# Kernel optimization log

Hardware: AMD Instinct MI355X
Metric: run time of the kernel (lower is better)

## Reference

```python
import jax, jax.numpy as jnp
import numpy as np
from jax import lax


def setup_inputs() -> dict:
    key = jax.random.key(0)
    x = jax.random.normal(key, (16, 3, 1024, 1024), dtype=jnp.float32)
    return {"x": x, "kernel_size": 7}


def _box_conv(x, kernel, pad):
    # x: (B,1,H,W), kernel: (1,1,k,k); 'same' spatial conv
    return lax.conv_general_dilated(
        x, kernel,
        window_strides=(1, 1),
        padding=[(pad, pad), (pad, pad)],
        dimension_numbers=("NCHW", "OIHW", "NCHW"),
    )


def reference(x, kernel_size):
    k = kernel_size
    pad = k // 2
    # ConvertToLuminance: for 4D input, x.dim()==4 -> channel mean (not RGB weights)
    lum = jnp.mean(x, axis=1, keepdims=True)  # (B,1,H,W)
    kernel = jnp.ones((1, 1, k, k), dtype=x.dtype) / (k * k)
    mean = _box_conv(lum, kernel, pad)
    sqr_mean = _box_conv(lum * lum, kernel, pad)
    var = sqr_mean - mean * mean
    return var
```

## Files before the change

### kernel.cpp

```cpp
#include <hip/hip_runtime.h>

#define Wd 1024
#define Hd 1024
#define SH 16
#define ITER (SH + 6)

__global__ __launch_bounds__(256, 4)
void lvm_stream(const float* __restrict__ x, float* __restrict__ out) {
    __shared__ __align__(16) float L[2][Wd + 8];

    const int b    = blockIdx.y;
    const int row0 = blockIdx.x * SH;
    const int tid  = threadIdx.x;
    const int c0   = tid * 4;

    const float* x0 = x + (size_t)b * 3 * Hd * Wd;
    const float* x1 = x0 + (size_t)Hd * Wd;
    const float* x2 = x1 + (size_t)Hd * Wd;
    float*       ob = out + (size_t)b * Hd * Wd;

    if (tid < 4) {
        L[0][tid] = 0.f; L[0][Wd + 4 + tid] = 0.f;
        L[1][tid] = 0.f; L[1][Wd + 4 + tid] = 0.f;
    }

    float4 ring1[7], ring2[7];

#pragma unroll
    for (int i = 0; i < ITER; ++i) {
        const int ri = row0 - 3 + i;
        float4 lum4 = make_float4(0.f, 0.f, 0.f, 0.f);
        if (ri >= 0 && ri < Hd) {
            size_t o = (size_t)ri * Wd + c0;
            float4 a = *(const float4*)(x0 + o);
            float4 g = *(const float4*)(x1 + o);
            float4 c = *(const float4*)(x2 + o);
            lum4.x = (a.x + g.x + c.x) * (1.f / 3.f);
            lum4.y = (a.y + g.y + c.y) * (1.f / 3.f);
            lum4.z = (a.z + g.z + c.z) * (1.f / 3.f);
            lum4.w = (a.w + g.w + c.w) * (1.f / 3.f);
        }
        float* Lr = L[i & 1];
        *(float4*)(Lr + 4 + c0) = lum4;
        __syncthreads();

        float4 va = *(const float4*)(Lr + c0);
        float4 vb = *(const float4*)(Lr + c0 + 4);
        float4 vc = *(const float4*)(Lr + c0 + 8);
        float v1 = va.y, v2 = va.z, v3 = va.w;
        float v4 = vb.x, v5 = vb.y, v6 = vb.z, v7 = vb.w;
        float v8 = vc.x, v9 = vc.y, v10 = vc.z;

        float s1a = v1 + v2 + v3 + v4 + v5 + v6 + v7;
        float s1b = s1a - v1 + v8;
        float s1c = s1b - v2 + v9;
        float s1d = s1c - v3 + v10;

        float q1 = v1 * v1, q2 = v2 * v2, q3 = v3 * v3, q4 = v4 * v4;
        float q5 = v5 * v5, q6 = v6 * v6, q7 = v7 * v7, q8 = v8 * v8;
        float q9 = v9 * v9, q10 = v10 * v10;
        float s2a = q1 + q2 + q3 + q4 + q5 + q6 + q7;
        float s2b = s2a - q1 + q8;
        float s2c = s2b - q2 + q9;
        float s2d = s2c - q3 + q10;

        ring1[i % 7] = make_float4(s1a, s1b, s1c, s1d);
        ring2[i % 7] = make_float4(s2a, s2b, s2c, s2d);

        if (i >= 6) {
            float4 t1 = ring1[0], t2 = ring2[0];
#pragma unroll
            for (int k = 1; k < 7; ++k) {
                t1.x += ring1[k].x; t1.y += ring1[k].y;
                t1.z += ring1[k].z; t1.w += ring1[k].w;
                t2.x += ring2[k].x; t2.y += ring2[k].y;
                t2.z += ring2[k].z; t2.w += ring2[k].w;
            }
            const float inv = 1.f / 49.f;
            float4 r;
            float mx = t1.x * inv, my = t1.y * inv, mz = t1.z * inv, mw = t1.w * inv;
            r.x = t2.x * inv - mx * mx;
            r.y = t2.y * inv - my * my;
            r.z = t2.z * inv - mz * mz;
            r.w = t2.w * inv - mw * mw;
            const int ro = row0 + i - 6;
            *(float4*)(ob + (size_t)ro * Wd + c0) = r;
        }
    }
}

extern "C" void kernel_launch(void* const* d_in, const int* in_sizes, int n_in,
                              void* d_out, int out_size, void* d_ws, size_t ws_size,
                              hipStream_t stream) {
    const float* x = (const float*)d_in[0];
    float* out = (float*)d_out;
    dim3 grid(Hd / SH, 16);
    lvm_stream<<<grid, dim3(256), 0, stream>>>(x, out);
}
```

Measured before the change: 302.3 us.

## Replace shared-memory row staging with wave shuffles and running vertical sum

Removes the LDS double buffer and per-row __syncthreads by getting horizontal neighbour luminance through wavefront shuffles. Lanes at wave edges reload the adjacent float4 from global memory to fill the halo. The vertical 7-row sum becomes a running add/subtract over the ring buffer instead of a full re-sum per output row. This drops barrier stalls and LDS traffic in a memory-bound kernel. In exchange it adds divergent edge loads and a slightly different floating-point accumulation order.

```diff
diff --git a/kernel.cpp b/kernel.cpp
--- a/kernel.cpp
+++ b/kernel.cpp
@@ -6,32 +6,31 @@
 #define ITER (SH + 6)
 
 __global__ __launch_bounds__(256, 4)
-void lvm_stream(const float* __restrict__ x, float* __restrict__ out) {
-    __shared__ __align__(16) float L[2][Wd + 8];
-
+void lvm_wave(const float* __restrict__ x, float* __restrict__ out) {
     const int b    = blockIdx.y;
     const int row0 = blockIdx.x * SH;
     const int tid  = threadIdx.x;
     const int c0   = tid * 4;
+    const int lane = tid & 63;
 
     const float* x0 = x + (size_t)b * 3 * Hd * Wd;
     const float* x1 = x0 + (size_t)Hd * Wd;
     const float* x2 = x1 + (size_t)Hd * Wd;
     float*       ob = out + (size_t)b * Hd * Wd;
 
-    if (tid < 4) {
-        L[0][tid] = 0.f; L[0][Wd + 4 + tid] = 0.f;
-        L[1][tid] = 0.f; L[1][Wd + 4 + tid] = 0.f;
-    }
-
     float4 ring1[7], ring2[7];
+    float4 t1 = make_float4(0.f, 0.f, 0.f, 0.f);
+    float4 t2 = make_float4(0.f, 0.f, 0.f, 0.f);
 
 #pragma unroll
     for (int i = 0; i < ITER; ++i) {
         const int ri = row0 - 3 + i;
         float4 lum4 = make_float4(0.f, 0.f, 0.f, 0.f);
+        float lm1 = 0.f, lm2 = 0.f, lm3 = 0.f;
+        float lp4 = 0.f, lp5 = 0.f, lp6 = 0.f;
+
         if (ri >= 0 && ri < Hd) {
-            size_t o = (size_t)ri * Wd + c0;
+            const size_t o = (size_t)ri * Wd + c0;
             float4 a = *(const float4*)(x0 + o);
             float4 g = *(const float4*)(x1 + o);
             float4 c = *(const float4*)(x2 + o);
@@ -39,46 +38,73 @@
             lum4.y = (a.y + g.y + c.y) * (1.f / 3.f);
             lum4.z = (a.z + g.z + c.z) * (1.f / 3.f);
             lum4.w = (a.w + g.w + c.w) * (1.f / 3.f);
+
+            lm1 = __shfl_up(lum4.y, 1);
+            lm2 = __shfl_up(lum4.z, 1);
+            lm3 = __shfl_up(lum4.w, 1);
+            lp4 = __shfl_down(lum4.x, 1);
+            lp5 = __shfl_down(lum4.y, 1);
+            lp6 = __shfl_down(lum4.z, 1);
+
+            if (lane == 0) {
+                if (c0 >= 4) {
+                    float4 a2 = *(const float4*)(x0 + o - 4);
+                    float4 g2 = *(const float4*)(x1 + o - 4);
+                    float4 c2 = *(const float4*)(x2 + o - 4);
+                    lm1 = (a2.y + g2.y + c2.y) * (1.f / 3.f);
+                    lm2 = (a2.z + g2.z + c2.z) * (1.f / 3.f);
+                    lm3 = (a2.w + g2.w + c2.w) * (1.f / 3.f);
+                } else {
+                    lm1 = lm2 = lm3 = 0.f;
+                }
+            }
+            if (lane == 63) {
+                if (c0 + 4 < Wd) {
+                    float4 a2 = *(const float4*)(x0 + o + 4);
+                    float4 g2 = *(const float4*)(x1 + o + 4);
+                    float4 c2 = *(const float4*)(x2 + o + 4);
+                    lp4 = (a2.x + g2.x + c2.x) * (1.f / 3.f);
+                    lp5 = (a2.y + g2.y + c2.y) * (1.f / 3.f);
+                    lp6 = (a2.z + g2.z + c2.z) * (1.f / 3.f);
+                } else {
+                    lp4 = lp5 = lp6 = 0.f;
+                }
+            }
         }
-        float* Lr = L[i & 1];
-        *(float4*)(Lr + 4 + c0) = lum4;
-        __syncthreads();
 
-        float4 va = *(const float4*)(Lr + c0);
-        float4 vb = *(const float4*)(Lr + c0 + 4);
-        float4 vc = *(const float4*)(Lr + c0 + 8);
-        float v1 = va.y, v2 = va.z, v3 = va.w;
-        float v4 = vb.x, v5 = vb.y, v6 = vb.z, v7 = vb.w;
-        float v8 = vc.x, v9 = vc.y, v10 = vc.z;
+        const float v1 = lm1, v2 = lm2, v3 = lm3;
+        const float v4 = lum4.x, v5 = lum4.y, v6 = lum4.z, v7 = lum4.w;
+        const float v8 = lp4, v9 = lp5, v10 = lp6;
 
         float s1a = v1 + v2 + v3 + v4 + v5 + v6 + v7;
         float s1b = s1a - v1 + v8;
         float s1c = s1b - v2 + v9;
         float s1d = s1c - v3 + v10;
 
-        float q1 = v1 * v1, q2 = v2 * v2, q3 = v3 * v3, q4 = v4 * v4;
-        float q5 = v5 * v5, q6 = v6 * v6, q7 = v7 * v7, q8 = v8 * v8;
-        float q9 = v9 * v9, q10 = v10 * v10;
+        float q1 = v1*v1, q2 = v2*v2, q3 = v3*v3, q4 = v4*v4, q5 = v5*v5;
+        float q6 = v6*v6, q7 = v7*v7, q8 = v8*v8, q9 = v9*v9, q10 = v10*v10;
         float s2a = q1 + q2 + q3 + q4 + q5 + q6 + q7;
         float s2b = s2a - q1 + q8;
         float s2c = s2b - q2 + q9;
         float s2d = s2c - q3 + q10;
 
-        ring1[i % 7] = make_float4(s1a, s1b, s1c, s1d);
-        ring2[i % 7] = make_float4(s2a, s2b, s2c, s2d);
+        float4 s1 = make_float4(s1a, s1b, s1c, s1d);
+        float4 s2 = make_float4(s2a, s2b, s2c, s2d);
+
+        t1.x += s1.x; t1.y += s1.y; t1.z += s1.z; t1.w += s1.w;
+        t2.x += s2.x; t2.y += s2.y; t2.z += s2.z; t2.w += s2.w;
+        if (i >= 7) {
+            float4 o1 = ring1[i % 7], o2 = ring2[i % 7];
+            t1.x -= o1.x; t1.y -= o1.y; t1.z -= o1.z; t1.w -= o1.w;
+            t2.x -= o2.x; t2.y -= o2.y; t2.z -= o2.z; t2.w -= o2.w;
+        }
+        ring1[i % 7] = s1;
+        ring2[i % 7] = s2;
 
         if (i >= 6) {
-            float4 t1 = ring1[0], t2 = ring2[0];
-#pragma unroll
-            for (int k = 1; k < 7; ++k) {
-                t1.x += ring1[k].x; t1.y += ring1[k].y;
-                t1.z += ring1[k].z; t1.w += ring1[k].w;
-                t2.x += ring2[k].x; t2.y += ring2[k].y;
-                t2.z += ring2[k].z; t2.w += ring2[k].w;
-            }
             const float inv = 1.f / 49.f;
+            float mx = t1.x * inv, my = t1.y * inv, mz = t1.z * inv, mw = t1.w * inv;
             float4 r;
-            float mx = t1.x * inv, my = t1.y * inv, mz = t1.z * inv, mw = t1.w * inv;
             r.x = t2.x * inv - mx * mx;
             r.y = t2.y * inv - my * my;
             r.z = t2.z * inv - mz * mz;
@@ -95,5 +121,5 @@
     const float* x = (const float*)d_in[0];
     float* out = (float*)d_out;
     dim3 grid(Hd / SH, 16);
-    lvm_stream<<<grid, dim3(256), 0, stream>>>(x, out);
+    lvm_wave<<<grid, dim3(256), 0, stream>>>(x, out);
 }
```

Measured after the change: 312.3 us. 1.03x slower.

## Replace shared-memory horizontal halo with per-thread overlapping float2 global loads

Applied to the files above, without the earlier changes.

Removes the shared-memory row buffer and its per-row __syncthreads. Each thread now covers two columns and reads its horizontal halo directly from global memory with five overlapping float2 loads per channel. The grid gains a column split, and the 1/3 channel scaling is folded into the final 1/147 and 1/441 constants. This trades barrier and LDS traffic for redundant global/L2 loads (about 2.5x the load instructions) and narrower vector accesses.

```diff
diff --git a/kernel.cpp b/kernel.cpp
--- a/kernel.cpp
+++ b/kernel.cpp
@@ -5,86 +5,88 @@
 #define SH 16
 #define ITER (SH + 6)
 
-__global__ __launch_bounds__(256, 4)
-void lvm_stream(const float* __restrict__ x, float* __restrict__ out) {
-    __shared__ __align__(16) float L[2][Wd + 8];
+__device__ __forceinline__ float2 ld2(const float* p) { return *(const float2*)p; }
 
-    const int b    = blockIdx.y;
+__global__ __launch_bounds__(256, 6)
+void lvm_f2(const float* __restrict__ x, float* __restrict__ out) {
+    const int b    = blockIdx.z;
     const int row0 = blockIdx.x * SH;
-    const int tid  = threadIdx.x;
-    const int c0   = tid * 4;
+    const int c0   = blockIdx.y * 512 + threadIdx.x * 2;
 
     const float* x0 = x + (size_t)b * 3 * Hd * Wd;
     const float* x1 = x0 + (size_t)Hd * Wd;
     const float* x2 = x1 + (size_t)Hd * Wd;
     float*       ob = out + (size_t)b * Hd * Wd;
 
-    if (tid < 4) {
-        L[0][tid] = 0.f; L[0][Wd + 4 + tid] = 0.f;
-        L[1][tid] = 0.f; L[1][Wd + 4 + tid] = 0.f;
+    int cofs[5];
+#pragma unroll
+    for (int j = 0; j < 5; ++j) {
+        int cl = c0 - 4 + 2 * j;
+        cofs[j] = min(max(cl, 0), Wd - 2);
     }
+    bool vld0 = (c0 - 3 >= 0), vld1 = (c0 - 2 >= 0), vld2 = (c0 - 1 >= 0);
+    bool vld5 = (c0 + 2 < Wd), vld6 = (c0 + 3 < Wd), vld7 = (c0 + 4 < Wd);
 
-    float4 ring1[7], ring2[7];
+    float2 ring1[7], ring2[7];
 
 #pragma unroll
     for (int i = 0; i < ITER; ++i) {
         const int ri = row0 - 3 + i;
-        float4 lum4 = make_float4(0.f, 0.f, 0.f, 0.f);
+        float2 A0, A1, A2, A3, A4;
         if (ri >= 0 && ri < Hd) {
-            size_t o = (size_t)ri * Wd + c0;
-            float4 a = *(const float4*)(x0 + o);
-            float4 g = *(const float4*)(x1 + o);
-            float4 c = *(const float4*)(x2 + o);
-            lum4.x = (a.x + g.x + c.x) * (1.f / 3.f);
-            lum4.y = (a.y + g.y + c.y) * (1.f / 3.f);
-            lum4.z = (a.z + g.z + c.z) * (1.f / 3.f);
-            lum4.w = (a.w + g.w + c.w) * (1.f / 3.f);
+            const size_t rb = (size_t)ri * Wd;
+            const float* p0 = x0 + rb;
+            const float* p1 = x1 + rb;
+            const float* p2 = x2 + rb;
+            float2 a, g, c;
+            a = ld2(p0 + cofs[0]); g = ld2(p1 + cofs[0]); c = ld2(p2 + cofs[0]);
+            A0 = make_float2(a.x + g.x + c.x, a.y + g.y + c.y);
+            a = ld2(p0 + cofs[1]); g = ld2(p1 + cofs[1]); c = ld2(p2 + cofs[1]);
+            A1 = make_float2(a.x + g.x + c.x, a.y + g.y + c.y);
+            a = ld2(p0 + cofs[2]); g = ld2(p1 + cofs[2]); c = ld2(p2 + cofs[2]);
+            A2 = make_float2(a.x + g.x + c.x, a.y + g.y + c.y);
+            a = ld2(p0 + cofs[3]); g = ld2(p1 + cofs[3]); c = ld2(p2 + cofs[3]);
+            A3 = make_float2(a.x + g.x + c.x, a.y + g.y + c.y);
+            a = ld2(p0 + cofs[4]); g = ld2(p1 + cofs[4]); c = ld2(p2 + cofs[4]);
+            A4 = make_float2(a.x + g.x + c.x, a.y + g.y + c.y);
+        } else {
+            A0 = A1 = A2 = A3 = A4 = make_float2(0.f, 0.f);
         }
-        float* Lr = L[i & 1];
-        *(float4*)(Lr + 4 + c0) = lum4;
-        __syncthreads();
 
-        float4 va = *(const float4*)(Lr + c0);
-        float4 vb = *(const float4*)(Lr + c0 + 4);
-        float4 vc = *(const float4*)(Lr + c0 + 8);
-        float v1 = va.y, v2 = va.z, v3 = va.w;
-        float v4 = vb.x, v5 = vb.y, v6 = vb.z, v7 = vb.w;
-        float v8 = vc.x, v9 = vc.y, v10 = vc.z;
+        float w0 = vld0 ? A0.y : 0.f;
+        float w1 = vld1 ? A1.x : 0.f;
+        float w2 = vld2 ? A1.y : 0.f;
+        float w3 = A2.x;
+        float w4 = A2.y;
+        float w5 = vld5 ? A3.x : 0.f;
+        float w6 = vld6 ? A3.y : 0.f;
+        float w7 = vld7 ? A4.x : 0.f;
 
-        float s1a = v1 + v2 + v3 + v4 + v5 + v6 + v7;
-        float s1b = s1a - v1 + v8;
-        float s1c = s1b - v2 + v9;
-        float s1d = s1c - v3 + v10;
+        float s1x = ((w0 + w1) + (w2 + w3)) + ((w4 + w5) + w6);
+        float s1y = s1x - w0 + w7;
+        float q0 = w0*w0, q1 = w1*w1, q2 = w2*w2, q3 = w3*w3;
+        float q4 = w4*w4, q5 = w5*w5, q6 = w6*w6, q7 = w7*w7;
+        float s2x = ((q0 + q1) + (q2 + q3)) + ((q4 + q5) + q6);
+        float s2y = s2x - q0 + q7;
 
-        float q1 = v1 * v1, q2 = v2 * v2, q3 = v3 * v3, q4 = v4 * v4;
-        float q5 = v5 * v5, q6 = v6 * v6, q7 = v7 * v7, q8 = v8 * v8;
-        float q9 = v9 * v9, q10 = v10 * v10;
-        float s2a = q1 + q2 + q3 + q4 + q5 + q6 + q7;
-        float s2b = s2a - q1 + q8;
-        float s2c = s2b - q2 + q9;
-        float s2d = s2c - q3 + q10;
-
-        ring1[i % 7] = make_float4(s1a, s1b, s1c, s1d);
-        ring2[i % 7] = make_float4(s2a, s2b, s2c, s2d);
+        ring1[i % 7] = make_float2(s1x, s1y);
+        ring2[i % 7] = make_float2(s2x, s2y);
 
         if (i >= 6) {
-            float4 t1 = ring1[0], t2 = ring2[0];
+            float2 t1 = ring1[0], t2 = ring2[0];
 #pragma unroll
             for (int k = 1; k < 7; ++k) {
                 t1.x += ring1[k].x; t1.y += ring1[k].y;
-                t1.z += ring1[k].z; t1.w += ring1[k].w;
                 t2.x += ring2[k].x; t2.y += ring2[k].y;
-                t2.z += ring2[k].z; t2.w += ring2[k].w;
             }
-            const float inv = 1.f / 49.f;
-            float4 r;
-            float mx = t1.x * inv, my = t1.y * inv, mz = t1.z * inv, mw = t1.w * inv;
-            r.x = t2.x * inv - mx * mx;
-            r.y = t2.y * inv - my * my;
-            r.z = t2.z * inv - mz * mz;
-            r.w = t2.w * inv - mw * mw;
+            const float inv1 = 1.f / 147.f;
+            const float inv2 = 1.f / 441.f;
+            float mx = t1.x * inv1, my = t1.y * inv1;
+            float2 r;
+            r.x = t2.x * inv2 - mx * mx;
+            r.y = t2.y * inv2 - my * my;
             const int ro = row0 + i - 6;
-            *(float4*)(ob + (size_t)ro * Wd + c0) = r;
+            *(float2*)(ob + (size_t)ro * Wd + c0) = r;
         }
     }
 }
@@ -94,6 +96,6 @@
                               hipStream_t stream) {
     const float* x = (const float*)d_in[0];
     float* out = (float*)d_out;
-    dim3 grid(Hd / SH, 16);
-    lvm_stream<<<grid, dim3(256), 0, stream>>>(x, out);
+    dim3 grid(Hd / SH, 2, 16);
+    lvm_f2<<<grid, dim3(256), 0, stream>>>(x, out);
 }
```

Result: slower. 353.6 us (+17.0%).

## Prefetch next row's loads, use running vertical sums and nontemporal stores

Applied to the files above, without the earlier changes.

Loads of the three channel rows for the next iteration are issued before the LDS barrier, so global latency overlaps the current row's compute. The 7-row vertical sum becomes a running sum (add new, subtract oldest) instead of re-summing the ring each row. The divide-by-3 is folded into the final scale constants, __syncthreads is replaced by a raw waitcnt+barrier, and outputs use nontemporal stores. The cost is more live registers for the prefetched values, plus small floating-point differences from the running-sum form.

```diff
diff --git a/kernel.cpp b/kernel.cpp
--- a/kernel.cpp
+++ b/kernel.cpp
@@ -5,8 +5,14 @@
 #define SH 16
 #define ITER (SH + 6)
 
+typedef float nfloat4 __attribute__((ext_vector_type(4)));
+
+__device__ __forceinline__ void sync_lds() {
+    asm volatile("s_waitcnt lgkmcnt(0)\n\ts_barrier" ::: "memory");
+}
+
 __global__ __launch_bounds__(256, 4)
-void lvm_stream(const float* __restrict__ x, float* __restrict__ out) {
+void lvm_pipe(const float* __restrict__ x, float* __restrict__ out) {
     __shared__ __align__(16) float L[2][Wd + 8];
 
     const int b    = blockIdx.y;
@@ -25,66 +31,93 @@
     }
 
     float4 ring1[7], ring2[7];
+    float4 t1 = make_float4(0.f, 0.f, 0.f, 0.f);
+    float4 t2 = make_float4(0.f, 0.f, 0.f, 0.f);
+
+    float4 pa, pg, pc;
+    bool pv;
+    {
+        const int ri = row0 - 3;
+        pv = (ri >= 0) && (ri < Hd);
+        if (pv) {
+            const size_t o = (size_t)ri * Wd + c0;
+            pa = *(const float4*)(x0 + o);
+            pg = *(const float4*)(x1 + o);
+            pc = *(const float4*)(x2 + o);
+        }
+    }
 
 #pragma unroll
     for (int i = 0; i < ITER; ++i) {
-        const int ri = row0 - 3 + i;
-        float4 lum4 = make_float4(0.f, 0.f, 0.f, 0.f);
-        if (ri >= 0 && ri < Hd) {
-            size_t o = (size_t)ri * Wd + c0;
-            float4 a = *(const float4*)(x0 + o);
-            float4 g = *(const float4*)(x1 + o);
-            float4 c = *(const float4*)(x2 + o);
-            lum4.x = (a.x + g.x + c.x) * (1.f / 3.f);
-            lum4.y = (a.y + g.y + c.y) * (1.f / 3.f);
-            lum4.z = (a.z + g.z + c.z) * (1.f / 3.f);
-            lum4.w = (a.w + g.w + c.w) * (1.f / 3.f);
+        float4 s;
+        if (pv) {
+            s.x = pa.x + pg.x + pc.x;
+            s.y = pa.y + pg.y + pc.y;
+            s.z = pa.z + pg.z + pc.z;
+            s.w = pa.w + pg.w + pc.w;
+        } else {
+            s = make_float4(0.f, 0.f, 0.f, 0.f);
         }
         float* Lr = L[i & 1];
-        *(float4*)(Lr + 4 + c0) = lum4;
-        __syncthreads();
+        *(float4*)(Lr + 4 + c0) = s;
+
+        if (i + 1 < ITER) {
+            const int ri = row0 - 3 + (i + 1);
+            pv = (ri >= 0) && (ri < Hd);
+            if (pv) {
+                const size_t o = (size_t)ri * Wd + c0;
+                pa = *(const float4*)(x0 + o);
+                pg = *(const float4*)(x1 + o);
+                pc = *(const float4*)(x2 + o);
+            }
+        }
+
+        sync_lds();
 
         float4 va = *(const float4*)(Lr + c0);
         float4 vb = *(const float4*)(Lr + c0 + 4);
         float4 vc = *(const float4*)(Lr + c0 + 8);
-        float v1 = va.y, v2 = va.z, v3 = va.w;
-        float v4 = vb.x, v5 = vb.y, v6 = vb.z, v7 = vb.w;
-        float v8 = vc.x, v9 = vc.y, v10 = vc.z;
+        const float v1 = va.y, v2 = va.z, v3 = va.w;
+        const float v4 = vb.x, v5 = vb.y, v6 = vb.z, v7 = vb.w;
+        const float v8 = vc.x, v9 = vc.y, v10 = vc.z;
 
-        float s1a = v1 + v2 + v3 + v4 + v5 + v6 + v7;
+        float s1a = ((v1 + v2) + (v3 + v4)) + ((v5 + v6) + v7);
         float s1b = s1a - v1 + v8;
         float s1c = s1b - v2 + v9;
         float s1d = s1c - v3 + v10;
 
-        float q1 = v1 * v1, q2 = v2 * v2, q3 = v3 * v3, q4 = v4 * v4;
-        float q5 = v5 * v5, q6 = v6 * v6, q7 = v7 * v7, q8 = v8 * v8;
-        float q9 = v9 * v9, q10 = v10 * v10;
-        float s2a = q1 + q2 + q3 + q4 + q5 + q6 + q7;
+        float q1 = v1*v1, q2 = v2*v2, q3 = v3*v3, q4 = v4*v4, q5 = v5*v5;
+        float q6 = v6*v6, q7 = v7*v7, q8 = v8*v8, q9 = v9*v9, q10 = v10*v10;
+        float s2a = ((q1 + q2) + (q3 + q4)) + ((q5 + q6) + q7);
         float s2b = s2a - q1 + q8;
         float s2c = s2b - q2 + q9;
         float s2d = s2c - q3 + q10;
 
-        ring1[i % 7] = make_float4(s1a, s1b, s1c, s1d);
-        ring2[i % 7] = make_float4(s2a, s2b, s2c, s2d);
+        float4 n1 = make_float4(s1a, s1b, s1c, s1d);
+        float4 n2 = make_float4(s2a, s2b, s2c, s2d);
+
+        t1.x += n1.x; t1.y += n1.y; t1.z += n1.z; t1.w += n1.w;
+        t2.x += n2.x; t2.y += n2.y; t2.z += n2.z; t2.w += n2.w;
+        if (i >= 7) {
+            float4 o1 = ring1[i % 7], o2 = ring2[i % 7];
+            t1.x -= o1.x; t1.y -= o1.y; t1.z -= o1.z; t1.w -= o1.w;
+            t2.x -= o2.x; t2.y -= o2.y; t2.z -= o2.z; t2.w -= o2.w;
+        }
+        ring1[i % 7] = n1;
+        ring2[i % 7] = n2;
 
         if (i >= 6) {
-            float4 t1 = ring1[0], t2 = ring2[0];
-#pragma unroll
-            for (int k = 1; k < 7; ++k) {
-                t1.x += ring1[k].x; t1.y += ring1[k].y;
-                t1.z += ring1[k].z; t1.w += ring1[k].w;
-                t2.x += ring2[k].x; t2.y += ring2[k].y;
-                t2.z += ring2[k].z; t2.w += ring2[k].w;
-            }
-            const float inv = 1.f / 49.f;
-            float4 r;
-            float mx = t1.x * inv, my = t1.y * inv, mz = t1.z * inv, mw = t1.w * inv;
-            r.x = t2.x * inv - mx * mx;
-            r.y = t2.y * inv - my * my;
-            r.z = t2.z * inv - mz * mz;
-            r.w = t2.w * inv - mw * mw;
+            const float inv1 = 1.f / 147.f;
+            const float inv2 = 1.f / 441.f;
+            float mx = t1.x * inv1, my = t1.y * inv1;
+            float mz = t1.z * inv1, mw = t1.w * inv1;
+            nfloat4 r;
+            r.x = t2.x * inv2 - mx * mx;
+            r.y = t2.y * inv2 - my * my;
+            r.z = t2.z * inv2 - mz * mz;
+            r.w = t2.w * inv2 - mw * mw;
             const int ro = row0 + i - 6;
-            *(float4*)(ob + (size_t)ro * Wd + c0) = r;
+            __builtin_nontemporal_store(r, (nfloat4*)(ob + (size_t)ro * Wd + c0));
         }
     }
 }
@@ -95,5 +128,5 @@
     const float* x = (const float*)d_in[0];
     float* out = (float*)d_out;
     dim3 grid(Hd / SH, 16);
-    lvm_stream<<<grid, dim3(256), 0, stream>>>(x, out);
+    lvm_pipe<<<grid, dim3(256), 0, stream>>>(x, out);
 }
```

Measured after the change: 303.4 us. About the same (+0.4%).
